# Kernel optimization log

Measured on AMD Instinct MI355X. Metric: run time of the kernel, lower is better.

## Reference

```python
import jax, jax.numpy as jnp
import numpy as np

N_NODES = 50000
N_EDGES = 800000
IN_DIM = 128
HID = 32
HEADS = 4
OUT_DIM = 64
NEG_SLOPE = 0.2  # DGL GATConv default


def setup_inputs() -> dict:
    key = jax.random.key(0)
    ks = jax.random.split(key, 20)

    def glorot(k, shape):
        fan = shape[0] + shape[-1]
        return (jax.random.normal(k, shape, jnp.float32) * np.sqrt(2.0 / fan)).astype(jnp.float32)

    inp = {
        "h": jax.random.normal(ks[0], (N_NODES, IN_DIM), jnp.float32),
        "src": jax.random.randint(ks[1], (N_EDGES,), 0, N_NODES, jnp.int32),
        "dst": jax.random.randint(ks[2], (N_EDGES,), 0, N_NODES, jnp.int32),
        # layer 0: in_dim -> hidden, HEADS heads, relu
        "W1": glorot(ks[3], (IN_DIM, HEADS * HID)),
        "al1": glorot(ks[4], (HEADS, HID)),
        "ar1": glorot(ks[5], (HEADS, HID)),
        "b1": jnp.zeros((HEADS * HID,), jnp.float32),
        # layer 1 (hidden): hidden*heads -> hidden, HEADS heads, relu
        "W2": glorot(ks[6], (HEADS * HID, HEADS * HID)),
        "al2": glorot(ks[7], (HEADS, HID)),
        "ar2": glorot(ks[8], (HEADS, HID)),
        "b2": jnp.zeros((HEADS * HID,), jnp.float32),
        # layer 2 (output): hidden*heads -> out_dim, 1 head, no activation
        "W3": glorot(ks[9], (HEADS * HID, OUT_DIM)),
        "al3": glorot(ks[10], (1, OUT_DIM)),
        "ar3": glorot(ks[11], (1, OUT_DIM)),
        "b3": jnp.zeros((OUT_DIM,), jnp.float32),
    }
    return inp


def gat_conv(h, src, dst, W, attn_l, attn_r, bias, heads, out_dim, use_relu):
    n = h.shape[0]
    feat = (h @ W).reshape(n, heads, out_dim)              # [N,H,D]
    el = jnp.sum(feat * attn_l[None], axis=-1)             # [N,H]
    er = jnp.sum(feat * attn_r[None], axis=-1)             # [N,H]
    e = jax.nn.leaky_relu(el[src] + er[dst], NEG_SLOPE)    # [E,H] per-edge logits
    # segment softmax over incoming edges of each dst node
    emax = jax.ops.segment_max(e, dst, num_segments=n)     # [N,H] (-inf for isolated nodes, never gathered)
    ee = jnp.exp(e - emax[dst])                            # [E,H]
    denom = jax.ops.segment_sum(ee, dst, num_segments=n)   # [N,H]
    alpha = ee / denom[dst]                                # [E,H]
    msg = feat[src] * alpha[:, :, None]                    # [E,H,D] gather + weight
    out = jax.ops.segment_sum(msg, dst, num_segments=n)    # [N,H,D] scatter-add
    out = out + bias.reshape(1, heads, out_dim)
    if use_relu:
        out = jax.nn.relu(out)
    return out.reshape(n, heads * out_dim)


def reference(h, src, dst, W1, al1, ar1, b1, W2, al2, ar2, b2, W3, al3, ar3, b3):
    # dropout is identity in eval mode
    h1 = gat_conv(h, src, dst, W1, al1, ar1, b1, HEADS, HID, True)
    h2 = gat_conv(h1, src, dst, W2, al2, ar2, b2, HEADS, HID, True)
    h3 = gat_conv(h2, src, dst, W3, al3, ar3, b3, 1, OUT_DIM, False)
    return h3
```

## Files before the change

### kernel.cpp

```cpp
#include <hip/hip_runtime.h>
#include <hip/hip_fp16.h>

#define NNODES 50000
#define NEDGES 800000

__device__ __forceinline__ float leaky(float x) { return x >= 0.f ? x : 0.2f * x; }

typedef _Float16 f16x8 __attribute__((ext_vector_type(8)));
typedef float f32x4 __attribute__((ext_vector_type(4)));

struct __align__(8)  half4v { __half2 h0, h1; };
struct __align__(16) half8v { __half2 h0, h1, h2, h3; };

template<int F, int H>
__global__ __launch_bounds__(256) void gemm_mfma_k(const float* __restrict__ X,
                                                   const float* __restrict__ W,
                                                   const float* __restrict__ al,
                                                   const float* __restrict__ ar,
                                                   __half* __restrict__ Yh,
                                                   float* __restrict__ el,
                                                   float* __restrict__ er, int n) {
    constexpr int K = 128;
    constexpr int ROWS = 64;
    constexpr int LDK = K + 8;
    constexpr int NT = F / 16;
    __shared__ __align__(16) __half Xs[ROWS * LDK];
    __shared__ __align__(16) __half Wt[F * LDK];

    const int tid = threadIdx.x;
    const int r0 = blockIdx.x * ROWS;

    for (int i = tid; i < ROWS * (K / 4); i += 256) {
        int r = i >> 5, c4 = i & 31;
        int row = r0 + r;
        float4 v = (row < n) ? ((const float4*)X)[(size_t)row * (K / 4) + c4]
                             : make_float4(0.f, 0.f, 0.f, 0.f);
        __half* d = &Xs[r * LDK + c4 * 4];
        d[0] = __float2half_rn(v.x); d[1] = __float2half_rn(v.y);
        d[2] = __float2half_rn(v.z); d[3] = __float2half_rn(v.w);
    }
    for (int i = tid; i < K * (F / 4); i += 256) {
        int k = i / (F / 4), n4 = i % (F / 4);
        float4 v = ((const float4*)W)[i];
        int nn = n4 * 4;
        Wt[(nn + 0) * LDK + k] = __float2half_rn(v.x);
        Wt[(nn + 1) * LDK + k] = __float2half_rn(v.y);
        Wt[(nn + 2) * LDK + k] = __float2half_rn(v.z);
        Wt[(nn + 3) * LDK + k] = __float2half_rn(v.w);
    }
    __syncthreads();

    const int wv = tid >> 6, lane = tid & 63;
    const int cl = lane & 15, kg = lane >> 4;

    f32x4 acc[NT];
    #pragma unroll
    for (int t = 0; t < NT; t++) acc[t] = (f32x4){0.f, 0.f, 0.f, 0.f};

    #pragma unroll
    for (int ks = 0; ks < K / 32; ks++) {
        f16x8 a = *(const f16x8*)&Xs[(16 * wv + cl) * LDK + ks * 32 + kg * 8];
        #pragma unroll
        for (int t = 0; t < NT; t++) {
            f16x8 b = *(const f16x8*)&Wt[(16 * t + cl) * LDK + ks * 32 + kg * 8];
            acc[t] = __builtin_amdgcn_mfma_f32_16x16x32_f16(a, b, acc[t], 0, 0, 0);
        }
    }

    #pragma unroll
    for (int t = 0; t < NT; t++)
        #pragma unroll
        for (int j = 0; j < 4; j++) {
            int row = r0 + 16 * wv + 4 * kg + j;
            if (row < n) Yh[(size_t)row * F + 16 * t + cl] = __float2half_rn(acc[t][j]);
        }

    float alv[NT], arv[NT];
    #pragma unroll
    for (int t = 0; t < NT; t++) { alv[t] = al[16 * t + cl]; arv[t] = ar[16 * t + cl]; }

    if (H == 1) {
        float pl[4], pr[4];
        #pragma unroll
        for (int j = 0; j < 4; j++) {
            pl[j] = 0.f; pr[j] = 0.f;
            #pragma unroll
            for (int t = 0; t < NT; t++) { pl[j] += acc[t][j] * alv[t]; pr[j] += acc[t][j] * arv[t]; }
        }
        #pragma unroll
        for (int off = 1; off < 16; off <<= 1)
            #pragma unroll
            for (int j = 0; j < 4; j++) { pl[j] += __shfl_xor(pl[j], off); pr[j] += __shfl_xor(pr[j], off); }
        if (cl == 0)
            #pragma unroll
            for (int j = 0; j < 4; j++) {
                int row = r0 + 16 * wv + 4 * kg + j;
                if (row < n) { el[row] = pl[j]; er[row] = pr[j]; }
            }
    } else {
        float pl[4][4], pr[4][4];
        #pragma unroll
        for (int hh = 0; hh < 4; hh++)
            #pragma unroll
            for (int j = 0; j < 4; j++) {
                pl[hh][j] = acc[2 * hh][j] * alv[2 * hh] + acc[2 * hh + 1][j] * alv[2 * hh + 1];
                pr[hh][j] = acc[2 * hh][j] * arv[2 * hh] + acc[2 * hh + 1][j] * arv[2 * hh + 1];
            }
        #pragma unroll
        for (int off = 1; off < 16; off <<= 1)
            #pragma unroll
            for (int hh = 0; hh < 4; hh++)
                #pragma unroll
                for (int j = 0; j < 4; j++) {
                    pl[hh][j] += __shfl_xor(pl[hh][j], off);
                    pr[hh][j] += __shfl_xor(pr[hh][j], off);
                }
        if (cl == 0)
            #pragma unroll
            for (int j = 0; j < 4; j++) {
                int row = r0 + 16 * wv + 4 * kg + j;
                if (row < n)
                    #pragma unroll
                    for (int hh = 0; hh < 4; hh++) {
                        el[row * 4 + hh] = pl[hh][j];
                        er[row * 4 + hh] = pr[hh][j];
                    }
            }
    }
}

__global__ void zero_k(int* __restrict__ cnt, int n) {
    int i = blockIdx.x * blockDim.x + threadIdx.x;
    if (i < n) cnt[i] = 0;
}

__global__ void hist_k(const int* __restrict__ dst, int* __restrict__ cnt,
                       int* __restrict__ rank) {
    int e = blockIdx.x * blockDim.x + threadIdx.x;
    if (e < NEDGES) rank[e] = atomicAdd(&cnt[dst[e]], 1);
}

__global__ void scan_blk_k(const int* __restrict__ cnt, int* __restrict__ offs,
                           int* __restrict__ bsum, int n) {
    __shared__ int sm[256];
    int tid = threadIdx.x;
    int i = blockIdx.x * 256 + tid;
    int v = (i < n) ? cnt[i] : 0;
    sm[tid] = v;
    __syncthreads();
    for (int off = 1; off < 256; off <<= 1) {
        int t = (tid >= off) ? sm[tid - off] : 0;
        __syncthreads();
        sm[tid] += t;
        __syncthreads();
    }
    if (i < n) offs[i] = sm[tid] - v;
    if (tid == 255) bsum[blockIdx.x] = sm[255];
}

__global__ void scan_top_k(int* __restrict__ bsum, int nb) {
    __shared__ int sm[256];
    int tid = threadIdx.x;
    int v = (tid < nb) ? bsum[tid] : 0;
    sm[tid] = v;
    __syncthreads();
    for (int off = 1; off < 256; off <<= 1) {
        int t = (tid >= off) ? sm[tid - off] : 0;
        __syncthreads();
        sm[tid] += t;
        __syncthreads();
    }
    if (tid < nb) bsum[tid] = sm[tid] - v;
}

__global__ void scan_add_k(int* __restrict__ offs, const int* __restrict__ bsum, int n) {
    int i = blockIdx.x * 256 + threadIdx.x;
    if (i < n) offs[i] += bsum[blockIdx.x];
    if (i == 0) offs[n] = NEDGES;
}

__global__ void scatter_k(const int* __restrict__ src, const int* __restrict__ dst,
                          const int* __restrict__ rank, const int* __restrict__ offs,
                          int* __restrict__ esrc) {
    int e = blockIdx.x * blockDim.x + threadIdx.x;
    if (e < NEDGES) esrc[offs[dst[e]] + rank[e]] = src[e];
}

template<bool RELU>
__global__ __launch_bounds__(256) void node_agg4_k(const int* __restrict__ offs,
                                                   const int* __restrict__ esrc,
                                                   const float* __restrict__ el,
                                                   const float* __restrict__ er,
                                                   const __half* __restrict__ feat,
                                                   const float* __restrict__ bias,
                                                   float* __restrict__ out) {
    int wid = (blockIdx.x * 256 + threadIdx.x) >> 6;
    int lane = threadIdx.x & 63;
    if (wid >= NNODES) return;
    int beg = offs[wid], end = offs[wid + 1];

    const int h  = lane & 3;
    const int q  = lane >> 4;
    const int cl = lane & 15;
    const int hd = cl >> 2;
    float erh = er[wid * 4 + h];

    float acc[8] = {0.f, 0.f, 0.f, 0.f, 0.f, 0.f, 0.f, 0.f};
    float dsum = 0.f;
    for (int base = beg; base < end; base += 16) {
        int rem = end - base;
        if (rem > 16) rem = 16;
        int sv = 0;
        if (lane < rem) sv = esrc[base + lane];
        int se = __shfl(sv, lane >> 2);
        float p = 0.f;
        if ((lane >> 2) < rem)
            p = __expf(leaky(el[se * 4 + h] + erh));
        dsum += p;
        #pragma unroll
        for (int e = 0; e < 16 && e < rem; e += 4) {
            int eidx = e + q;
            int s = __shfl(sv, eidx);
            float a = __shfl(p, eidx * 4 + hd);
            half8v hv = *(const half8v*)&feat[(size_t)s * 128 + 8 * cl];
            float2 f0 = __half22float2(hv.h0);
            float2 f1 = __half22float2(hv.h1);
            float2 f2 = __half22float2(hv.h2);
            float2 f3 = __half22float2(hv.h3);
            acc[0] += f0.x * a; acc[1] += f0.y * a;
            acc[2] += f1.x * a; acc[3] += f1.y * a;
            acc[4] += f2.x * a; acc[5] += f2.y * a;
            acc[6] += f3.x * a; acc[7] += f3.y * a;
        }
    }
    #pragma unroll
    for (int c = 0; c < 8; c++) {
        acc[c] += __shfl_xor(acc[c], 16);
        acc[c] += __shfl_xor(acc[c], 32);
    }
    #pragma unroll
    for (int off = 4; off < 64; off <<= 1) dsum += __shfl_xor(dsum, off);
    float dh = __shfl(dsum, hd);
    float inv = dh > 0.f ? 1.f / dh : 0.f;
    if (q == 0) {
        float4 ba = *(const float4*)&bias[8 * cl];
        float4 bb = *(const float4*)&bias[8 * cl + 4];
        float v0 = acc[0] * inv + ba.x, v1 = acc[1] * inv + ba.y;
        float v2 = acc[2] * inv + ba.z, v3 = acc[3] * inv + ba.w;
        float v4 = acc[4] * inv + bb.x, v5 = acc[5] * inv + bb.y;
        float v6 = acc[6] * inv + bb.z, v7 = acc[7] * inv + bb.w;
        if (RELU) {
            v0 = fmaxf(v0, 0.f); v1 = fmaxf(v1, 0.f); v2 = fmaxf(v2, 0.f); v3 = fmaxf(v3, 0.f);
            v4 = fmaxf(v4, 0.f); v5 = fmaxf(v5, 0.f); v6 = fmaxf(v6, 0.f); v7 = fmaxf(v7, 0.f);
        }
        *(float4*)&out[(size_t)wid * 128 + 8 * cl]     = make_float4(v0, v1, v2, v3);
        *(float4*)&out[(size_t)wid * 128 + 8 * cl + 4] = make_float4(v4, v5, v6, v7);
    }
}

__global__ __launch_bounds__(256) void node_agg1_k(const int* __restrict__ offs,
                                                   const int* __restrict__ esrc,
                                                   const float* __restrict__ el,
                                                   const float* __restrict__ er,
                                                   const __half* __restrict__ feat,
                                                   const float* __restrict__ bias,
                                                   float* __restrict__ out) {
    int wid = (blockIdx.x * 256 + threadIdx.x) >> 6;
    int lane = threadIdx.x & 63;
    if (wid >= NNODES) return;
    int beg = offs[wid], end = offs[wid + 1];

    const int q  = lane >> 4;
    const int cl = lane & 15;
    float erd = er[wid];

    float acc[4] = {0.f, 0.f, 0.f, 0.f};
    float dsum = 0.f;
    for (int base = beg; base < end; base += 64) {
        int rem = end - base;
        if (rem > 64) rem = 64;
        int sv = 0;
        float p = 0.f;
        if (lane < rem) {
            sv = esrc[base + lane];
            p = __expf(leaky(el[sv] + erd));
        }
        dsum += p;
        #pragma unroll 4
        for (int e = 0; e < rem; e += 4) {
            int eidx = e + q;
            int s = __shfl(sv, eidx);
            float a = __shfl(p, eidx);
            half4v hv = *(const half4v*)&feat[(size_t)s * 64 + 4 * cl];
            float2 f0 = __half22float2(hv.h0);
            float2 f1 = __half22float2(hv.h1);
            acc[0] += f0.x * a; acc[1] += f0.y * a;
            acc[2] += f1.x * a; acc[3] += f1.y * a;
        }
    }
    #pragma unroll
    for (int c = 0; c < 4; c++) {
        acc[c] += __shfl_xor(acc[c], 16);
        acc[c] += __shfl_xor(acc[c], 32);
    }
    #pragma unroll
    for (int off = 1; off < 64; off <<= 1) dsum += __shfl_xor(dsum, off);
    float inv = dsum > 0.f ? 1.f / dsum : 0.f;
    if (q == 0) {
        float4 b4 = *(const float4*)&bias[4 * cl];
        *(float4*)&out[(size_t)wid * 64 + 4 * cl] =
            make_float4(acc[0] * inv + b4.x, acc[1] * inv + b4.y,
                        acc[2] * inv + b4.z, acc[3] * inv + b4.w);
    }
}

extern "C" void kernel_launch(void* const* d_in, const int* in_sizes, int n_in,
                              void* d_out, int out_size, void* d_ws, size_t ws_size,
                              hipStream_t stream) {
    const float* h   = (const float*)d_in[0];
    const int*   src = (const int*)d_in[1];
    const int*   dst = (const int*)d_in[2];
    const float* W1  = (const float*)d_in[3];
    const float* al1 = (const float*)d_in[4];
    const float* ar1 = (const float*)d_in[5];
    const float* b1  = (const float*)d_in[6];
    const float* W2  = (const float*)d_in[7];
    const float* al2 = (const float*)d_in[8];
    const float* ar2 = (const float*)d_in[9];
    const float* b2  = (const float*)d_in[10];
    const float* W3  = (const float*)d_in[11];
    const float* al3 = (const float*)d_in[12];
    const float* ar3 = (const float*)d_in[13];
    const float* b3  = (const float*)d_in[14];
    float* out = (float*)d_out;

    const int n = NNODES;
    __half* feat16 = (__half*)d_ws;
    float*  hbuf   = (float*)(feat16 + (size_t)n * 128);
    float*  el     = hbuf + (size_t)n * 128;
    float*  er     = el + (size_t)n * 4;
    int*    cnt    = (int*)(er + (size_t)n * 4);
    int*    offs   = cnt + n;
    int*    esrc   = offs + (n + 1);
    int*    bsum   = esrc + NEDGES;
    int*    rank   = (int*)hbuf;

    const int gemmBlocks = (n + 63) / 64;
    const int nBlk = (n + 255) / 256;
    const int eBlk = (NEDGES + 255) / 256;
    const int waveBlk = (n + 3) / 4;

    zero_k<<<nBlk, 256, 0, stream>>>(cnt, n);
    hist_k<<<eBlk, 256, 0, stream>>>(dst, cnt, rank);
    scan_blk_k<<<nBlk, 256, 0, stream>>>(cnt, offs, bsum, n);
    scan_top_k<<<1, 256, 0, stream>>>(bsum, nBlk);
    scan_add_k<<<nBlk, 256, 0, stream>>>(offs, bsum, n);
    scatter_k<<<eBlk, 256, 0, stream>>>(src, dst, rank, offs, esrc);

    gemm_mfma_k<128, 4><<<gemmBlocks, 256, 0, stream>>>(h, W1, al1, ar1, feat16, el, er, n);
    node_agg4_k<true><<<waveBlk, 256, 0, stream>>>(offs, esrc, el, er, feat16, b1, hbuf);

    gemm_mfma_k<128, 4><<<gemmBlocks, 256, 0, stream>>>(hbuf, W2, al2, ar2, feat16, el, er, n);
    node_agg4_k<true><<<waveBlk, 256, 0, stream>>>(offs, esrc, el, er, feat16, b2, hbuf);

    gemm_mfma_k<64, 1><<<gemmBlocks, 256, 0, stream>>>(hbuf, W3, al3, ar3, feat16, el, er, n);
    node_agg1_k<<<waveBlk, 256, 0, stream>>>(offs, esrc, el, er, feat16, b3, out);
}
```

Baseline: 244.0 us.

## Store hidden activations in fp16 and use grid-stride persistent aggregation waves

The aggregation kernels now write hidden-layer outputs as fp16 rather than fp32, and the next GEMM loads those fp16 tiles directly instead of loading floats and converting them. This halves the traffic for the intermediate activations. The aggregation kernels also switch from one wave per node over about 12.5k blocks to a fixed grid of 2048 blocks looping grid-stride over nodes, with the bias loaded once per wave. The results differ slightly because the stored activations are rounded to fp16, though the GEMM was already converting them to fp16.

Measured after the change: 233.3 us. 1.05x faster.

```diff
diff --git a/kernel.cpp b/kernel.cpp
--- a/kernel.cpp
+++ b/kernel.cpp
@@ -12,8 +12,8 @@
 struct __align__(8)  half4v { __half2 h0, h1; };
 struct __align__(16) half8v { __half2 h0, h1, h2, h3; };
 
-template<int F, int H>
-__global__ __launch_bounds__(256) void gemm_mfma_k(const float* __restrict__ X,
+template<int F, int H, bool FP16IN>
+__global__ __launch_bounds__(256) void gemm_mfma_k(const void* __restrict__ Xv,
                                                    const float* __restrict__ W,
                                                    const float* __restrict__ al,
                                                    const float* __restrict__ ar,
@@ -30,14 +30,28 @@
     const int tid = threadIdx.x;
     const int r0 = blockIdx.x * ROWS;
 
-    for (int i = tid; i < ROWS * (K / 4); i += 256) {
-        int r = i >> 5, c4 = i & 31;
-        int row = r0 + r;
-        float4 v = (row < n) ? ((const float4*)X)[(size_t)row * (K / 4) + c4]
-                             : make_float4(0.f, 0.f, 0.f, 0.f);
-        __half* d = &Xs[r * LDK + c4 * 4];
-        d[0] = __float2half_rn(v.x); d[1] = __float2half_rn(v.y);
-        d[2] = __float2half_rn(v.z); d[3] = __float2half_rn(v.w);
+    if constexpr (FP16IN) {
+        const __half* X = (const __half*)Xv;
+        for (int i = tid; i < ROWS * (K / 8); i += 256) {
+            int r = i >> 4, c8 = i & 15;
+            int row = r0 + r;
+            half8v v;
+            __half2 z = __halves2half2(__float2half_rn(0.f), __float2half_rn(0.f));
+            v.h0 = z; v.h1 = z; v.h2 = z; v.h3 = z;
+            if (row < n) v = ((const half8v*)X)[(size_t)row * (K / 8) + c8];
+            *(half8v*)&Xs[r * LDK + c8 * 8] = v;
+        }
+    } else {
+        const float* X = (const float*)Xv;
+        for (int i = tid; i < ROWS * (K / 4); i += 256) {
+            int r = i >> 5, c4 = i & 31;
+            int row = r0 + r;
+            float4 v = (row < n) ? ((const float4*)X)[(size_t)row * (K / 4) + c4]
+                                 : make_float4(0.f, 0.f, 0.f, 0.f);
+            __half* d = &Xs[r * LDK + c4 * 4];
+            d[0] = __float2half_rn(v.x); d[1] = __float2half_rn(v.y);
+            d[2] = __float2half_rn(v.z); d[3] = __float2half_rn(v.w);
+        }
     }
     for (int i = tid; i < K * (F / 4); i += 256) {
         int k = i / (F / 4), n4 = i % (F / 4);
@@ -186,75 +200,79 @@
     if (e < NEDGES) esrc[offs[dst[e]] + rank[e]] = src[e];
 }
 
-template<bool RELU>
 __global__ __launch_bounds__(256) void node_agg4_k(const int* __restrict__ offs,
                                                    const int* __restrict__ esrc,
                                                    const float* __restrict__ el,
                                                    const float* __restrict__ er,
                                                    const __half* __restrict__ feat,
                                                    const float* __restrict__ bias,
-                                                   float* __restrict__ out) {
-    int wid = (blockIdx.x * 256 + threadIdx.x) >> 6;
-    int lane = threadIdx.x & 63;
-    if (wid >= NNODES) return;
-    int beg = offs[wid], end = offs[wid + 1];
+                                                   __half* __restrict__ out) {
+    const int lane = threadIdx.x & 63;
+    const int gw0 = (blockIdx.x * 256 + threadIdx.x) >> 6;
+    const int NW = (gridDim.x * 256) >> 6;
 
     const int h  = lane & 3;
     const int q  = lane >> 4;
     const int cl = lane & 15;
     const int hd = cl >> 2;
-    float erh = er[wid * 4 + h];
-
-    float acc[8] = {0.f, 0.f, 0.f, 0.f, 0.f, 0.f, 0.f, 0.f};
-    float dsum = 0.f;
-    for (int base = beg; base < end; base += 16) {
-        int rem = end - base;
-        if (rem > 16) rem = 16;
-        int sv = 0;
-        if (lane < rem) sv = esrc[base + lane];
-        int se = __shfl(sv, lane >> 2);
-        float p = 0.f;
-        if ((lane >> 2) < rem)
-            p = __expf(leaky(el[se * 4 + h] + erh));
-        dsum += p;
-        #pragma unroll
-        for (int e = 0; e < 16 && e < rem; e += 4) {
-            int eidx = e + q;
-            int s = __shfl(sv, eidx);
-            float a = __shfl(p, eidx * 4 + hd);
-            half8v hv = *(const half8v*)&feat[(size_t)s * 128 + 8 * cl];
-            float2 f0 = __half22float2(hv.h0);
-            float2 f1 = __half22float2(hv.h1);
-            float2 f2 = __half22float2(hv.h2);
-            float2 f3 = __half22float2(hv.h3);
-            acc[0] += f0.x * a; acc[1] += f0.y * a;
-            acc[2] += f1.x * a; acc[3] += f1.y * a;
-            acc[4] += f2.x * a; acc[5] += f2.y * a;
-            acc[6] += f3.x * a; acc[7] += f3.y * a;
-        }
-    }
-    #pragma unroll
-    for (int c = 0; c < 8; c++) {
-        acc[c] += __shfl_xor(acc[c], 16);
-        acc[c] += __shfl_xor(acc[c], 32);
-    }
-    #pragma unroll
-    for (int off = 4; off < 64; off <<= 1) dsum += __shfl_xor(dsum, off);
-    float dh = __shfl(dsum, hd);
-    float inv = dh > 0.f ? 1.f / dh : 0.f;
-    if (q == 0) {
-        float4 ba = *(const float4*)&bias[8 * cl];
-        float4 bb = *(const float4*)&bias[8 * cl + 4];
-        float v0 = acc[0] * inv + ba.x, v1 = acc[1] * inv + ba.y;
-        float v2 = acc[2] * inv + ba.z, v3 = acc[3] * inv + ba.w;
-        float v4 = acc[4] * inv + bb.x, v5 = acc[5] * inv + bb.y;
-        float v6 = acc[6] * inv + bb.z, v7 = acc[7] * inv + bb.w;
-        if (RELU) {
-            v0 = fmaxf(v0, 0.f); v1 = fmaxf(v1, 0.f); v2 = fmaxf(v2, 0.f); v3 = fmaxf(v3, 0.f);
-            v4 = fmaxf(v4, 0.f); v5 = fmaxf(v5, 0.f); v6 = fmaxf(v6, 0.f); v7 = fmaxf(v7, 0.f);
-        }
-        *(float4*)&out[(size_t)wid * 128 + 8 * cl]     = make_float4(v0, v1, v2, v3);
-        *(float4*)&out[(size_t)wid * 128 + 8 * cl + 4] = make_float4(v4, v5, v6, v7);
+
+    float4 ba, bb;
+    ba = *(const float4*)&bias[8 * cl];
+    bb = *(const float4*)&bias[8 * cl + 4];
+
+    for (int wid = gw0; wid < NNODES; wid += NW) {
+        int beg = offs[wid], end = offs[wid + 1];
+        float erh = er[wid * 4 + h];
+
+        float acc[8] = {0.f, 0.f, 0.f, 0.f, 0.f, 0.f, 0.f, 0.f};
+        float dsum = 0.f;
+        for (int base = beg; base < end; base += 16) {
+            int rem = end - base;
+            if (rem > 16) rem = 16;
+            int sv = 0;
+            if (lane < rem) sv = esrc[base + lane];
+            int se = __shfl(sv, lane >> 2);
+            float p = 0.f;
+            if ((lane >> 2) < rem)
+                p = __expf(leaky(el[se * 4 + h] + erh));
+            dsum += p;
+            #pragma unroll
+            for (int e = 0; e < 16 && e < rem; e += 4) {
+                int eidx = e + q;
+                int s = __shfl(sv, eidx);
+                float a = __shfl(p, eidx * 4 + hd);
+                half8v hv = *(const half8v*)&feat[(size_t)s * 128 + 8 * cl];
+                float2 f0 = __half22float2(hv.h0);
+                float2 f1 = __half22float2(hv.h1);
+                float2 f2 = __half22float2(hv.h2);
+                float2 f3 = __half22float2(hv.h3);
+                acc[0] += f0.x * a; acc[1] += f0.y * a;
+                acc[2] += f1.x * a; acc[3] += f1.y * a;
+                acc[4] += f2.x * a; acc[5] += f2.y * a;
+                acc[6] += f3.x * a; acc[7] += f3.y * a;
+            }
+        }
+        #pragma unroll
+        for (int c = 0; c < 8; c++) {
+            acc[c] += __shfl_xor(acc[c], 16);
+            acc[c] += __shfl_xor(acc[c], 32);
+        }
+        #pragma unroll
+        for (int off = 4; off < 64; off <<= 1) dsum += __shfl_xor(dsum, off);
+        float dh = __shfl(dsum, hd);
+        float inv = dh > 0.f ? 1.f / dh : 0.f;
+        if (q == 0) {
+            float v0 = fmaxf(acc[0] * inv + ba.x, 0.f), v1 = fmaxf(acc[1] * inv + ba.y, 0.f);
+            float v2 = fmaxf(acc[2] * inv + ba.z, 0.f), v3 = fmaxf(acc[3] * inv + ba.w, 0.f);
+            float v4 = fmaxf(acc[4] * inv + bb.x, 0.f), v5 = fmaxf(acc[5] * inv + bb.y, 0.f);
+            float v6 = fmaxf(acc[6] * inv + bb.z, 0.f), v7 = fmaxf(acc[7] * inv + bb.w, 0.f);
+            half8v hv;
+            hv.h0 = __halves2half2(__float2half_rn(v0), __float2half_rn(v1));
+            hv.h1 = __halves2half2(__float2half_rn(v2), __float2half_rn(v3));
+            hv.h2 = __halves2half2(__float2half_rn(v4), __float2half_rn(v5));
+            hv.h3 = __halves2half2(__float2half_rn(v6), __float2half_rn(v7));
+            *(half8v*)&out[(size_t)wid * 128 + 8 * cl] = hv;
+        }
     }
 }
 
@@ -265,52 +283,55 @@
                                                    const __half* __restrict__ feat,
                                                    const float* __restrict__ bias,
                                                    float* __restrict__ out) {
-    int wid = (blockIdx.x * 256 + threadIdx.x) >> 6;
-    int lane = threadIdx.x & 63;
-    if (wid >= NNODES) return;
-    int beg = offs[wid], end = offs[wid + 1];
+    const int lane = threadIdx.x & 63;
+    const int gw0 = (blockIdx.x * 256 + threadIdx.x) >> 6;
+    const int NW = (gridDim.x * 256) >> 6;
 
     const int q  = lane >> 4;
     const int cl = lane & 15;
-    float erd = er[wid];
-
-    float acc[4] = {0.f, 0.f, 0.f, 0.f};
-    float dsum = 0.f;
-    for (int base = beg; base < end; base += 64) {
-        int rem = end - base;
-        if (rem > 64) rem = 64;
-        int sv = 0;
-        float p = 0.f;
-        if (lane < rem) {
-            sv = esrc[base + lane];
-            p = __expf(leaky(el[sv] + erd));
-        }
-        dsum += p;
-        #pragma unroll 4
-        for (int e = 0; e < rem; e += 4) {
-            int eidx = e + q;
-            int s = __shfl(sv, eidx);
-            float a = __shfl(p, eidx);
-            half4v hv = *(const half4v*)&feat[(size_t)s * 64 + 4 * cl];
-            float2 f0 = __half22float2(hv.h0);
-            float2 f1 = __half22float2(hv.h1);
-            acc[0] += f0.x * a; acc[1] += f0.y * a;
-            acc[2] += f1.x * a; acc[3] += f1.y * a;
-        }
-    }
-    #pragma unroll
-    for (int c = 0; c < 4; c++) {
-        acc[c] += __shfl_xor(acc[c], 16);
-        acc[c] += __shfl_xor(acc[c], 32);
-    }
-    #pragma unroll
-    for (int off = 1; off < 64; off <<= 1) dsum += __shfl_xor(dsum, off);
-    float inv = dsum > 0.f ? 1.f / dsum : 0.f;
-    if (q == 0) {
-        float4 b4 = *(const float4*)&bias[4 * cl];
-        *(float4*)&out[(size_t)wid * 64 + 4 * cl] =
-            make_float4(acc[0] * inv + b4.x, acc[1] * inv + b4.y,
-                        acc[2] * inv + b4.z, acc[3] * inv + b4.w);
+    float4 b4 = *(const float4*)&bias[4 * cl];
+
+    for (int wid = gw0; wid < NNODES; wid += NW) {
+        int beg = offs[wid], end = offs[wid + 1];
+        float erd = er[wid];
+
+        float acc[4] = {0.f, 0.f, 0.f, 0.f};
+        float dsum = 0.f;
+        for (int base = beg; base < end; base += 64) {
+            int rem = end - base;
+            if (rem > 64) rem = 64;
+            int sv = 0;
+            float p = 0.f;
+            if (lane < rem) {
+                sv = esrc[base + lane];
+                p = __expf(leaky(el[sv] + erd));
+            }
+            dsum += p;
+            #pragma unroll 4
+            for (int e = 0; e < rem; e += 4) {
+                int eidx = e + q;
+                int s = __shfl(sv, eidx);
+                float a = __shfl(p, eidx);
+                half4v hv = *(const half4v*)&feat[(size_t)s * 64 + 4 * cl];
+                float2 f0 = __half22float2(hv.h0);
+                float2 f1 = __half22float2(hv.h1);
+                acc[0] += f0.x * a; acc[1] += f0.y * a;
+                acc[2] += f1.x * a; acc[3] += f1.y * a;
+            }
+        }
+        #pragma unroll
+        for (int c = 0; c < 4; c++) {
+            acc[c] += __shfl_xor(acc[c], 16);
+            acc[c] += __shfl_xor(acc[c], 32);
+        }
+        #pragma unroll
+        for (int off = 1; off < 64; off <<= 1) dsum += __shfl_xor(dsum, off);
+        float inv = dsum > 0.f ? 1.f / dsum : 0.f;
+        if (q == 0) {
+            *(float4*)&out[(size_t)wid * 64 + 4 * cl] =
+                make_float4(acc[0] * inv + b4.x, acc[1] * inv + b4.y,
+                            acc[2] * inv + b4.z, acc[3] * inv + b4.w);
+        }
     }
 }
 
@@ -336,19 +357,19 @@
 
     const int n = NNODES;
     __half* feat16 = (__half*)d_ws;
-    float*  hbuf   = (float*)(feat16 + (size_t)n * 128);
-    float*  el     = hbuf + (size_t)n * 128;
+    __half* hbuf16 = feat16 + (size_t)n * 128;
+    float*  el     = (float*)(hbuf16 + (size_t)n * 128);
     float*  er     = el + (size_t)n * 4;
     int*    cnt    = (int*)(er + (size_t)n * 4);
     int*    offs   = cnt + n;
     int*    esrc   = offs + (n + 1);
     int*    bsum   = esrc + NEDGES;
-    int*    rank   = (int*)hbuf;
+    int*    rank   = (int*)feat16;
 
     const int gemmBlocks = (n + 63) / 64;
     const int nBlk = (n + 255) / 256;
     const int eBlk = (NEDGES + 255) / 256;
-    const int waveBlk = (n + 3) / 4;
+    const int aggBlk = 2048;
 
     zero_k<<<nBlk, 256, 0, stream>>>(cnt, n);
     hist_k<<<eBlk, 256, 0, stream>>>(dst, cnt, rank);
@@ -357,12 +378,12 @@
     scan_add_k<<<nBlk, 256, 0, stream>>>(offs, bsum, n);
     scatter_k<<<eBlk, 256, 0, stream>>>(src, dst, rank, offs, esrc);
 
-    gemm_mfma_k<128, 4><<<gemmBlocks, 256, 0, stream>>>(h, W1, al1, ar1, feat16, el, er, n);
-    node_agg4_k<true><<<waveBlk, 256, 0, stream>>>(offs, esrc, el, er, feat16, b1, hbuf);
-
-    gemm_mfma_k<128, 4><<<gemmBlocks, 256, 0, stream>>>(hbuf, W2, al2, ar2, feat16, el, er, n);
-    node_agg4_k<true><<<waveBlk, 256, 0, stream>>>(offs, esrc, el, er, feat16, b2, hbuf);
-
-    gemm_mfma_k<64, 1><<<gemmBlocks, 256, 0, stream>>>(hbuf, W3, al3, ar3, feat16, el, er, n);
-    node_agg1_k<<<waveBlk, 256, 0, stream>>>(offs, esrc, el, er, feat16, b3, out);
-}
+    gemm_mfma_k<128, 4, false><<<gemmBlocks, 256, 0, stream>>>(h, W1, al1, ar1, feat16, el, er, n);
+    node_agg4_k<<<aggBlk, 256, 0, stream>>>(offs, esrc, el, er, feat16, b1, hbuf16);
+
+    gemm_mfma_k<128, 4, true><<<gemmBlocks, 256, 0, stream>>>(hbuf16, W2, al2, ar2, feat16, el, er, n);
+    node_agg4_k<<<aggBlk, 256, 0, stream>>>(offs, esrc, el, er, feat16, b2, hbuf16);
+
+    gemm_mfma_k<64, 1, true><<<gemmBlocks, 256, 0, stream>>>(hbuf16, W3, al3, ar3, feat16, el, er, n);
+    node_agg1_k<<<aggBlk, 256, 0, stream>>>(offs, esrc, el, er, feat16, b3, out);
+}
```
